# Kernel optimization log

Hardware: AMD Instinct MI355X
Metric: run time of the kernel (lower is better)

## Reference

```python
import jax, jax.numpy as jnp
import numpy as np

FEAT_STRIDE = 16
SCALES = np.array([8.0, 16.0, 32.0])
RATIOS = np.array([0.5, 1.0, 2.0])
PRE_NMS_TOP_N = 6000
POST_NMS_TOP_N = 300
NMS_THRESH = 0.7


def _whctrs(anchor):
    w = anchor[2] - anchor[0] + 1.0
    h = anchor[3] - anchor[1] + 1.0
    cx = anchor[0] + 0.5 * (w - 1.0)
    cy = anchor[1] + 0.5 * (h - 1.0)
    return w, h, cx, cy


def _mkanchors(ws, hs, cx, cy):
    return np.stack([cx - 0.5 * (ws - 1.0), cy - 0.5 * (hs - 1.0),
                     cx + 0.5 * (ws - 1.0), cy + 0.5 * (hs - 1.0)], axis=1)


def generate_anchors(base_size=16, ratios=RATIOS, scales=SCALES):
    base = np.array([0.0, 0.0, base_size - 1.0, base_size - 1.0])
    w, h, cx, cy = _whctrs(base)
    size = w * h
    ws = np.round(np.sqrt(size / ratios))
    hs = np.round(ws * ratios)
    ratio_anchors = _mkanchors(ws, hs, cx, cy)
    out = []
    for a in ratio_anchors:
        w, h, cx, cy = _whctrs(a)
        out.append(_mkanchors(w * scales, h * scales, cx, cy))
    return np.vstack(out)  # (A=9, 4)


def setup_inputs():
    key = jax.random.key(0)
    k1, k2 = jax.random.split(key)
    B, A, H, W = 8, 9, 152, 152
    scores_in = jax.random.normal(k1, (B, 2 * A, H, W), jnp.float32)
    bbox_deltas = 0.5 * jax.random.normal(k2, (B, 4 * A, H, W), jnp.float32)
    im_info = jnp.tile(jnp.array([[H * FEAT_STRIDE, W * FEAT_STRIDE, 1.0]], jnp.float32), (B, 1))
    anchors = jnp.asarray(generate_anchors(), jnp.float32)
    return {"scores_in": scores_in, "bbox_deltas": bbox_deltas, "im_info": im_info, "anchors": anchors}


def bbox_transform_inv(boxes, deltas):
    w = boxes[..., 2] - boxes[..., 0] + 1.0
    h = boxes[..., 3] - boxes[..., 1] + 1.0
    cx = boxes[..., 0] + 0.5 * w
    cy = boxes[..., 1] + 0.5 * h
    dx, dy, dw, dh = deltas[..., 0], deltas[..., 1], deltas[..., 2], deltas[..., 3]
    pcx = dx * w + cx
    pcy = dy * h + cy
    pw = jnp.exp(dw) * w
    ph = jnp.exp(dh) * h
    return jnp.stack([pcx - 0.5 * pw, pcy - 0.5 * ph, pcx + 0.5 * pw, pcy + 0.5 * ph], axis=-1)


def clip_boxes(boxes, im_info):
    wmax = im_info[:, None, 1] - 1.0  # x bound, per image
    hmax = im_info[:, None, 0] - 1.0  # y bound
    x1 = jnp.minimum(jnp.maximum(boxes[..., 0], 0.0), wmax)
    y1 = jnp.minimum(jnp.maximum(boxes[..., 1], 0.0), hmax)
    x2 = jnp.minimum(jnp.maximum(boxes[..., 2], 0.0), wmax)
    y2 = jnp.minimum(jnp.maximum(boxes[..., 3], 0.0), hmax)
    return jnp.stack([x1, y1, x2, y2], axis=-1)


def nms_indices(boxes, thresh, max_out):
    # boxes: (N, 4), sorted by score descending. Greedy NMS -> up to max_out indices, -1 padded.
    x1, y1, x2, y2 = boxes[:, 0], boxes[:, 1], boxes[:, 2], boxes[:, 3]
    areas = (x2 - x1 + 1.0) * (y2 - y1 + 1.0)
    N = boxes.shape[0]

    def body(i, carry):
        suppressed, keep = carry
        idx = jnp.argmax(~suppressed)  # first surviving box = highest remaining score
        valid = ~suppressed[idx]
        keep = keep.at[i].set(jnp.where(valid, idx.astype(jnp.int32), -1))
        xx1 = jnp.maximum(x1[idx], x1)
        yy1 = jnp.maximum(y1[idx], y1)
        xx2 = jnp.minimum(x2[idx], x2)
        yy2 = jnp.minimum(y2[idx], y2)
        inter = jnp.maximum(xx2 - xx1 + 1.0, 0.0) * jnp.maximum(yy2 - yy1 + 1.0, 0.0)
        iou = inter / (areas[idx] + areas - inter)
        suppressed = jnp.where(valid, suppressed | (iou > thresh), suppressed)
        return suppressed, keep

    _, keep = jax.lax.fori_loop(0, max_out, body,
                                (jnp.zeros(N, bool), jnp.full(max_out, -1, jnp.int32)))
    return keep


def _forward(scores_in, bbox_deltas, im_info, anchors):
    B, _, H, W = scores_in.shape
    A = anchors.shape[0]
    # fg objectness scores: channels [A:2A] -> (B, K*A) in (row, col, anchor) order
    scores = scores_in[:, A:].transpose(0, 2, 3, 1).reshape(B, -1)
    deltas = bbox_deltas.transpose(0, 2, 3, 1).reshape(B, -1, 4)
    sx = (jnp.arange(W) * FEAT_STRIDE).astype(jnp.float32)
    sy = (jnp.arange(H) * FEAT_STRIDE).astype(jnp.float32)
    gx, gy = jnp.meshgrid(sx, sy)  # (H, W)
    shifts = jnp.stack([gx.ravel(), gy.ravel(), gx.ravel(), gy.ravel()], axis=1)  # (K, 4)
    all_anchors = (anchors[None, :, :] + shifts[:, None, :]).reshape(-1, 4)  # (K*A, 4)
    proposals = bbox_transform_inv(all_anchors[None], deltas)  # (B, K*A, 4)
    proposals = clip_boxes(proposals, im_info)
    _, order = jax.lax.top_k(scores, PRE_NMS_TOP_N)  # descending, == sorted order truncated
    props_top = jnp.take_along_axis(proposals, order[..., None], axis=1)  # (B, PRE, 4)
    keep = jax.vmap(lambda b: nms_indices(b, NMS_THRESH, POST_NMS_TOP_N))(props_top)  # (B, POST)
    valid = keep >= 0
    sel = jnp.take_along_axis(props_top, jnp.maximum(keep, 0)[..., None], axis=1)
    sel = jnp.where(valid[..., None], sel, 0.0)
    batch_col = jnp.broadcast_to(jnp.arange(B, dtype=jnp.float32)[:, None, None],
                                 (B, POST_NMS_TOP_N, 1))
    return jnp.concatenate([batch_col, sel], axis=2)  # (B, POST, 5)


def reference(scores_in, bbox_deltas, im_info, anchors):
    return _forward(scores_in, bbox_deltas, im_info, anchors)
```

## Files before the change

### kernel.cpp

```cpp
#include <hip/hip_runtime.h>
#include <stdint.h>

#define H_ 152
#define W_ 152
#define A_ 9
#define HW_ (H_ * W_)
#define N_ (HW_ * A_)
#define B_ 8
#define PRE_TOP 6000
#define POST_TOP 300
#define NBUCK 4096
#define NFINE 32768
#define CAND_CAP 8192
#define NMS_TH 0.7f
#define CNT_STRIDE 32
#define RTILE 512
#define DEC_PIXBLK 91
#define DEC_BLKS (72 * DEC_PIXBLK)
#define ZERO_BLKS 128

#define OFF_HIST    0
#define OFF_SSUF    131072
#define OFF_CNT     262144
#define OFF_CAND    263168
#define OFF_GROUP   787456
#define OFF_BOXES   1311744
#define OFF_BALL    2079744
#define WS_NEED     (2079744ull + 26615808ull)


__device__ __forceinline__ unsigned fkey(float f) {
    unsigned u = __float_as_uint(f);
    return (u & 0x80000000u) ? ~u : (u | 0x80000000u);
}

__device__ __forceinline__ bool sup_test(float ax1, float ay1, float ax2, float ay2, float aar,
                                         float bx1, float by1, float bx2, float by2, float bar) {
    float xx1 = fmaxf(ax1, bx1);
    float yy1 = fmaxf(ay1, by1);
    float xx2 = fminf(ax2, bx2);
    float yy2 = fminf(ay2, by2);
    float iw = fmaxf(xx2 - xx1 + 1.0f, 0.0f);
    float ih = fmaxf(yy2 - yy1 + 1.0f, 0.0f);
    float inter = __fmul_rn(iw, ih);
    float iou = inter / (aar + bar - inter);
    return iou > NMS_TH;
}

__device__ __forceinline__ float4 decode_box(float an0, float an1, float an2, float an3,
                                             float sx, float sy,
                                             float dx, float dy, float dw, float dh,
                                             float wmax, float hmax) {
    float ax1 = an0 + sx;
    float ay1 = an1 + sy;
    float ax2 = an2 + sx;
    float ay2 = an3 + sy;
    float ww = ax2 - ax1 + 1.0f;
    float hh = ay2 - ay1 + 1.0f;
    float ctx = ax1 + 0.5f * ww;
    float cty = ay1 + 0.5f * hh;
    float pcx = __fadd_rn(__fmul_rn(dx, ww), ctx);
    float pcy = __fadd_rn(__fmul_rn(dy, hh), cty);
    float pw = __fmul_rn(expf(dw), ww);
    float ph = __fmul_rn(expf(dh), hh);
    float x1 = pcx - 0.5f * pw;
    float y1 = pcy - 0.5f * ph;
    float x2 = pcx + 0.5f * pw;
    float y2 = pcy + 0.5f * ph;
    x1 = fminf(fmaxf(x1, 0.0f), wmax);
    y1 = fminf(fmaxf(y1, 0.0f), hmax);
    x2 = fminf(fmaxf(x2, 0.0f), wmax);
    y2 = fminf(fmaxf(y2, 0.0f), hmax);
    return make_float4(x1, y1, x2, y2);
}


__global__ void init_k(const float* __restrict__ deltas,
                       const float* __restrict__ anchors,
                       const float* __restrict__ im_info,
                       float4* __restrict__ ball,
                       unsigned* __restrict__ zbase, unsigned* __restrict__ zboxes,
                       int nDecBlks) {
    int bid = blockIdx.x;
    if (bid < nDecBlks) {
        int ba = bid / DEC_PIXBLK;
        int b = ba / A_, a = ba - (ba / A_) * A_;
        int pix = (bid % DEC_PIXBLK) * 256 + threadIdx.x;
        if (pix >= HW_) return;
        const float* db = deltas + ((size_t)b * 36 + 4 * a) * HW_;
        float dx = db[pix];
        float dy = db[pix + HW_];
        float dw = db[pix + 2 * HW_];
        float dh = db[pix + 3 * HW_];
        float an0 = anchors[a * 4 + 0];
        float an1 = anchors[a * 4 + 1];
        float an2 = anchors[a * 4 + 2];
        float an3 = anchors[a * 4 + 3];
        float hmax = im_info[b * 3 + 0] - 1.0f;
        float wmax = im_info[b * 3 + 1] - 1.0f;
        int w = pix % W_, h = pix / W_;
        float sx = (float)(w * 16), sy = (float)(h * 16);
        ball[(size_t)b * N_ + a * HW_ + pix] =
            decode_box(an0, an1, an2, an3, sx, sy, dx, dy, dw, dh, wmax, hmax);
    } else {
        const int n1 = 263168 / 4;
        const int n2 = 768000 / 4;
        int i = (bid - nDecBlks) * 256 + (int)threadIdx.x;
        int st = ZERO_BLKS * 256;
        for (int k = i; k < n1 + n2; k += st) {
            if (k < n1) zbase[k] = 0u;
            else zboxes[k - n1] = 0u;
        }
    }
}

__global__ void hist_k(const float* __restrict__ scores, unsigned* __restrict__ hist) {
    __shared__ unsigned lh[NBUCK];
    int b = blockIdx.y;
    for (int i = threadIdx.x; i < NBUCK; i += blockDim.x) lh[i] = 0;
    __syncthreads();
    const float4* sb = (const float4*)(scores + ((size_t)b * 18 + A_) * HW_);
    const int N4 = N_ / 4;
    int stride = gridDim.x * blockDim.x;
    for (int e = blockIdx.x * blockDim.x + threadIdx.x; e < N4; e += stride) {
        float4 v = sb[e];
        atomicAdd(&lh[fkey(v.x) >> 20], 1u);
        atomicAdd(&lh[fkey(v.y) >> 20], 1u);
        atomicAdd(&lh[fkey(v.z) >> 20], 1u);
        atomicAdd(&lh[fkey(v.w) >> 20], 1u);
    }
    __syncthreads();
    for (int i = threadIdx.x; i < NBUCK; i += blockDim.x) {
        unsigned v = lh[i];
        if (v) atomicAdd(&hist[b * NBUCK + i], v);
    }
}

__global__ void scan_k(const unsigned* __restrict__ hist, unsigned* __restrict__ bucketT) {
    __shared__ unsigned ps[1024];
    int b = blockIdx.x, t = threadIdx.x;
    const unsigned* hb = hist + b * NBUCK;
    unsigned c0 = hb[4095 - (4 * t + 0)];
    unsigned c1 = hb[4095 - (4 * t + 1)];
    unsigned c2 = hb[4095 - (4 * t + 2)];
    unsigned c3 = hb[4095 - (4 * t + 3)];
    unsigned local = c0 + c1 + c2 + c3;
    ps[t] = local;
    __syncthreads();
    for (int off = 1; off < 1024; off <<= 1) {
        unsigned v = (t >= off) ? ps[t - off] : 0u;
        __syncthreads();
        ps[t] += v;
        __syncthreads();
    }
    unsigned incl = ps[t], excl = incl - local;
    if (excl < PRE_TOP && incl >= PRE_TOP) {
        unsigned cum = excl;
        unsigned cc[4] = {c0, c1, c2, c3};
#pragma unroll
        for (int k = 0; k < 4; ++k) {
            cum += cc[k];
            if (cum >= PRE_TOP) { bucketT[b] = (unsigned)(4095 - (4 * t + k)); break; }
        }
    }
    if (t == 1023 && ps[1023] < PRE_TOP) bucketT[b] = 0;
}

__global__ void compact_k(const float* __restrict__ scores, const unsigned* __restrict__ bucketT,
                          unsigned* __restrict__ cnt, uint2* __restrict__ cand) {
    __shared__ unsigned wtot[4], wbase[4];
    __shared__ unsigned blkbase;
    int b = blockIdx.y;
    const float4* sb = (const float4*)(scores + ((size_t)b * 18 + A_) * HW_);
    unsigned T = bucketT[b];
    int lane = threadIdx.x & 63;
    int wid = threadIdx.x >> 6;
    const int N4 = N_ / 4;
    int stride = gridDim.x * blockDim.x;
    int niters = (N4 + stride - 1) / stride;
    unsigned long long lower = (lane == 63) ? 0x7fffffffffffffffull
                                            : ((1ull << lane) - 1ull);
    for (int it = 0; it < niters; ++it) {
        int e = it * stride + blockIdx.x * (int)blockDim.x + (int)threadIdx.x;
        bool p0 = false, p1 = false, p2 = false, p3 = false;
        unsigned k0 = 0, k1 = 0, k2 = 0, k3 = 0;
        if (e < N4) {
            float4 v = sb[e];
            k0 = fkey(v.x); k1 = fkey(v.y); k2 = fkey(v.z); k3 = fkey(v.w);
            p0 = (k0 >> 20) >= T; p1 = (k1 >> 20) >= T;
            p2 = (k2 >> 20) >= T; p3 = (k3 >> 20) >= T;
        }
        unsigned long long m0 = __ballot(p0), m1 = __ballot(p1);
        unsigned long long m2 = __ballot(p2), m3 = __ballot(p3);
        unsigned t0 = (unsigned)__popcll(m0), t1 = (unsigned)__popcll(m1);
        unsigned t2 = (unsigned)__popcll(m2), t3 = (unsigned)__popcll(m3);
        unsigned wtotal = t0 + t1 + t2 + t3;
        if (lane == 0) wtot[wid] = wtotal;
        __syncthreads();
        if (threadIdx.x == 0) {
            unsigned s0 = wtot[0], s1 = wtot[1], s2 = wtot[2], s3 = wtot[3];
            unsigned tot = s0 + s1 + s2 + s3;
            blkbase = tot ? atomicAdd(&cnt[b * CNT_STRIDE], tot) : 0u;
            wbase[0] = 0; wbase[1] = s0; wbase[2] = s0 + s1; wbase[3] = s0 + s1 + s2;
        }
        __syncthreads();
        if (wtotal) {
            unsigned base = blkbase + wbase[wid];
            unsigned o0 = base + (unsigned)__popcll(m0 & lower);
            unsigned o1 = base + t0 + (unsigned)__popcll(m1 & lower);
            unsigned o2 = base + t0 + t1 + (unsigned)__popcll(m2 & lower);
            unsigned o3 = base + t0 + t1 + t2 + (unsigned)__popcll(m3 & lower);
            uint2* cb = cand + (size_t)b * CAND_CAP;
            int e4 = e * 4;
            if (p0 && o0 < CAND_CAP) {
                int a = (e4 + 0) / HW_, pix = (e4 + 0) - a * HW_;
                cb[o0] = make_uint2(k0, (unsigned)(pix * A_ + a));
            }
            if (p1 && o1 < CAND_CAP) {
                int a = (e4 + 1) / HW_, pix = (e4 + 1) - a * HW_;
                cb[o1] = make_uint2(k1, (unsigned)(pix * A_ + a));
            }
            if (p2 && o2 < CAND_CAP) {
                int a = (e4 + 2) / HW_, pix = (e4 + 2) - a * HW_;
                cb[o2] = make_uint2(k2, (unsigned)(pix * A_ + a));
            }
            if (p3 && o3 < CAND_CAP) {
                int a = (e4 + 3) / HW_, pix = (e4 + 3) - a * HW_;
                cb[o3] = make_uint2(k3, (unsigned)(pix * A_ + a));
            }
        }
    }
}

__global__ void __launch_bounds__(1024) finesort_k(const unsigned* __restrict__ cnt,
                                                   uint2* __restrict__ cand,
                                                   unsigned long long* __restrict__ grouped) {
    __shared__ unsigned lh[NFINE];
    __shared__ unsigned ps[1024];
    int b = blockIdx.x, t = threadIdx.x;
    int M = min((int)cnt[b * CNT_STRIDE], CAND_CAP);
    uint2* cb = cand + (size_t)b * CAND_CAP;
    unsigned long long* g = grouped + (size_t)b * CAND_CAP;
    for (int i = t; i < NFINE; i += 1024) lh[i] = 0u;
    __syncthreads();
    for (int i = t; i < M; i += 1024) {
        unsigned key16 = cb[i].x >> 16;
        unsigned f = (key16 >= 32768u) ? (key16 - 32768u) : 0u;
        atomicAdd(&lh[f], 1u);
    }
    __syncthreads();
    unsigned c[32];
    unsigned local = 0;
#pragma unroll
    for (int k = 0; k < 32; ++k) { c[k] = lh[32767 - (32 * t + k)]; local += c[k]; }
    ps[t] = local;
    __syncthreads();
    for (int off = 1; off < 1024; off <<= 1) {
        unsigned v = (t >= off) ? ps[t - off] : 0u;
        __syncthreads();
        ps[t] += v;
        __syncthreads();
    }
    unsigned run = ps[t] - local;
    __syncthreads();
#pragma unroll
    for (int k = 0; k < 32; ++k) {
        lh[32767 - (32 * t + k)] = run;
        run += c[k];
    }
    __syncthreads();
    for (int i = t; i < M; i += 1024) {
        uint2 cd = cb[i];
        unsigned key16 = cd.x >> 16;
        unsigned f = (key16 >= 32768u) ? (key16 - 32768u) : 0u;
        unsigned pos = atomicAdd(&lh[f], 1u);
        if (pos < CAND_CAP)
            g[pos] = ((unsigned long long)cd.x << 32) | (unsigned)(~cd.y);
    }
    __syncthreads();
    ushort* S16 = (ushort*)cb;
    for (int i = t; i < NFINE; i += 1024)
        S16[i] = (ushort)min(lh[i], 65535u);
}

__global__ void __launch_bounds__(256) rank_k(const unsigned* __restrict__ cnt,
                                              const unsigned long long* __restrict__ grouped,
                                              const ushort* __restrict__ S16all,
                                              const float* __restrict__ deltas,
                                              const float* __restrict__ anchors,
                                              const float* __restrict__ im_info,
                                              const float4* __restrict__ ball,
                                              float4* __restrict__ boxes) {
    __shared__ unsigned long long tile[RTILE];
    __shared__ int s_rs, s_re;
    int b = blockIdx.y, t = threadIdx.x;
    int M = min((int)cnt[b * CNT_STRIDE], CAND_CAP);
    int c0 = blockIdx.x * 256;
    if (c0 >= M) return;
    const unsigned long long* g = grouped + (size_t)b * CAND_CAP;
    const ushort* S16 = S16all + (size_t)b * NFINE;
    int i = c0 + t;
    bool valid = i < M;
    unsigned long long comp = valid ? g[i] : 0ull;

    unsigned n = valid ? ~(unsigned)comp : 0u;
    int a = (int)(n % A_);
    int pix = (int)(n / A_);

    float4 pre = make_float4(0.f, 0.f, 0.f, 0.f);
    float dx = 0.f, dy = 0.f, dw = 0.f, dh = 0.f;
    float an0 = 0.f, an1 = 0.f, an2 = 0.f, an3 = 0.f, hmax = 0.f, wmax = 0.f;
    if (ball) {
        if (valid) pre = ball[(size_t)b * N_ + a * HW_ + pix];
    } else if (valid) {
        const float* db = deltas + (size_t)b * 36 * HW_;
        int didx = (4 * a) * HW_ + pix;
        dx = db[didx];
        dy = db[didx + HW_];
        dw = db[didx + 2 * HW_];
        dh = db[didx + 3 * HW_];
        an0 = anchors[a * 4 + 0];
        an1 = anchors[a * 4 + 1];
        an2 = anchors[a * 4 + 2];
        an3 = anchors[a * 4 + 3];
        hmax = im_info[b * 3 + 0] - 1.0f;
        wmax = im_info[b * 3 + 1] - 1.0f;
    }

    unsigned key16 = (unsigned)(comp >> 48);
    int f = (key16 >= 32768u) ? (int)(key16 - 32768u) : 0;
    int bs = 0, be = 0;
    if (valid) {
        bs = (f < 32767) ? min((int)S16[f + 1], M) : 0;
        be = min((int)S16[f], M);
    }
    if (t == 0) {
        unsigned kf = (unsigned)(g[c0] >> 48);
        int bf = (kf >= 32768u) ? (int)(kf - 32768u) : 0;
        int last = min(c0 + 255, M - 1);
        unsigned kl = (unsigned)(g[last] >> 48);
        int bl = (kl >= 32768u) ? (int)(kl - 32768u) : 0;
        s_rs = (bf < 32767) ? min((int)S16[bf + 1], M) : 0;
        s_re = min((int)S16[bl], M);
    }
    __syncthreads();
    int rs = s_rs, re = s_re;
    int cgt = 0;
    for (int tb = rs; tb < re; tb += RTILE) {
        int navail = min(RTILE, re - tb);
        __syncthreads();
        for (int j = t; j < navail; j += 256) tile[j] = g[tb + j];
        __syncthreads();
        if (valid) {
            int lo = max(bs, tb) - tb;
            int hi = min(be, tb + navail) - tb;
            int a0 = 0, a1 = 0, a2 = 0, a3 = 0, a4 = 0, a5 = 0, a6 = 0, a7 = 0;
            int j = lo;
            for (; j + 8 <= hi; j += 8) {
                unsigned long long v0 = tile[j + 0];
                unsigned long long v1 = tile[j + 1];
                unsigned long long v2 = tile[j + 2];
                unsigned long long v3 = tile[j + 3];
                unsigned long long v4 = tile[j + 4];
                unsigned long long v5 = tile[j + 5];
                unsigned long long v6 = tile[j + 6];
                unsigned long long v7 = tile[j + 7];
                a0 += (v0 > comp); a1 += (v1 > comp); a2 += (v2 > comp); a3 += (v3 > comp);
                a4 += (v4 > comp); a5 += (v5 > comp); a6 += (v6 > comp); a7 += (v7 > comp);
            }
            for (; j < hi; ++j) cgt += (tile[j] > comp);
            cgt += (a0 + a1 + a2 + a3) + (a4 + a5 + a6 + a7);
        }
    }
    if (!valid) return;
    int rank = bs + cgt;
    if (rank >= PRE_TOP) return;

    float4 result;
    if (ball) {
        result = pre;
    } else {
        int w = pix % W_, h = pix / W_;
        float sx = (float)(w * 16), sy = (float)(h * 16);
        result = decode_box(an0, an1, an2, an3, sx, sy, dx, dy, dw, dh, wmax, hmax);
    }
    boxes[(size_t)b * PRE_TOP + rank] = result;
}

__global__ void __launch_bounds__(1024) nms_k(const float4* __restrict__ boxes,
                                              float* __restrict__ out) {
    __shared__ float4 kbox[POST_TOP];
    __shared__ float  karea[POST_TOP];
    __shared__ float4 gbox4[64];
    __shared__ float  gar[64];
    __shared__ unsigned extw[2];
    __shared__ unsigned intraw[128];
    __shared__ unsigned long long s_keep;
    __shared__ int s_base, s_kc, s_done;
    int b = blockIdx.x, t = threadIdx.x;
    int lane = t & 63, w = t >> 6;
    if (t == 0) { s_kc = 0; s_done = 0; }
    const float4* bb = boxes + (size_t)b * PRE_TOP;
    const int ngroups = (PRE_TOP + 63) / 64;

    float4 vcur = make_float4(0.f, 0.f, 0.f, 0.f);
    if (t < 64) vcur = bb[t];

    for (int g = 0; g < ngroups; ++g) {
        __syncthreads();
        if (s_done) break;
        int gbase = g * 64;
        int gsz = min(64, PRE_TOP - gbase);
        if (t < gsz) {
            gbox4[t] = vcur;
            gar[t] = __fmul_rn(vcur.z - vcur.x + 1.0f, vcur.w - vcur.y + 1.0f);
        }
        if (t < 64) {
            int nidx = min(gbase + 64 + t, PRE_TOP - 1);
            vcur = bb[nidx];
        }
        if (t < 2) extw[t] = 0u;
        if (t < 128) intraw[t] = 0u;
        __syncthreads();

        int kc = s_kc;
        {
            int j = t >> 4, sub = t & 15;
            if (j < gsz) {
                float4 cb4 = gbox4[j];
                float car = gar[j];
                bool any = false;
                for (int kk = sub; kk < kc && !any; kk += 16) {
                    float4 kb = kbox[kk];
                    float ka = karea[kk];
                    any = sup_test(kb.x, kb.y, kb.z, kb.w, ka,
                                   cb4.x, cb4.y, cb4.z, cb4.w, car);
                }
                if (any) atomicOr(&extw[j >> 5], 1u << (j & 31));
            }
        }
        {
            float4 mb = gbox4[lane];
            float mar = gar[lane];
#pragma unroll
            for (int it = 0; it < 4; ++it) {
                int jj = w + it * 16;
                float4 bj = gbox4[jj];
                float baj = gar[jj];
                bool sup = (jj < lane) && (lane < gsz) && (jj < gsz) &&
                           sup_test(bj.x, bj.y, bj.z, bj.w, baj,
                                    mb.x, mb.y, mb.z, mb.w, mar);
                unsigned long long m = __ballot(sup);
                if (lane == 0 && (unsigned)m) atomicOr(&intraw[2 * jj], (unsigned)m);
                if (lane == 1 && (unsigned)(m >> 32))
                    atomicOr(&intraw[2 * jj + 1], (unsigned)(m >> 32));
            }
        }
        __syncthreads();

        if (t == 0) {
            unsigned long long ext64 = (unsigned long long)extw[0] |
                                       ((unsigned long long)extw[1] << 32);
            unsigned long long validm = (gsz >= 64) ? ~0ull : ((1ull << gsz) - 1ull);
            unsigned long long alive = (~ext64) & validm;
            unsigned long long keep = 0ull;
            int kcc = s_kc;
            s_base = kcc;
            while (alive && kcc < POST_TOP) {
                int j = __ffsll((long long)alive) - 1;
                keep |= (1ull << j);
                ++kcc;
                unsigned long long row = (unsigned long long)intraw[2 * j] |
                                         ((unsigned long long)intraw[2 * j + 1] << 32);
                alive &= ~row;
                alive &= ~(1ull << j);
            }
            s_keep = keep;
            s_kc = kcc;
            if (kcc >= POST_TOP) s_done = 1;
        }
        __syncthreads();

        if (t < gsz && ((s_keep >> t) & 1ull)) {
            int rank = __popcll(s_keep & ((1ull << t) - 1ull));
            int slot = s_base + rank;
            float4 mb = gbox4[t];
            kbox[slot] = mb;
            karea[slot] = gar[t];
            float* o = out + (size_t)(b * POST_TOP + slot) * 5;
            o[0] = (float)b; o[1] = mb.x; o[2] = mb.y; o[3] = mb.z; o[4] = mb.w;
        }
    }
    __syncthreads();
    for (int sl = s_kc + t; sl < POST_TOP; sl += 1024) {
        float* o = out + (size_t)(b * POST_TOP + sl) * 5;
        o[0] = (float)b; o[1] = 0.f; o[2] = 0.f; o[3] = 0.f; o[4] = 0.f;
    }
}


extern "C" void kernel_launch(void* const* d_in, const int* in_sizes, int n_in,
                              void* d_out, int out_size, void* d_ws, size_t ws_size,
                              hipStream_t stream) {
    const float* scores  = (const float*)d_in[0];
    const float* deltas  = (const float*)d_in[1];
    const float* im_info = (const float*)d_in[2];
    const float* anchors = (const float*)d_in[3];
    float* out = (float*)d_out;

    unsigned*           hist    = (unsigned*)((char*)d_ws + OFF_HIST);
    unsigned*           cnt     = (unsigned*)((char*)d_ws + OFF_CNT);
    uint2*              cand    = (uint2*)((char*)d_ws + OFF_CAND);
    unsigned long long* grouped = (unsigned long long*)((char*)d_ws + OFF_GROUP);
    float4*             boxes   = (float4*)((char*)d_ws + OFF_BOXES);
    unsigned*           bucketT = cnt + B_ * CNT_STRIDE - 8;

    bool useBall = ws_size >= WS_NEED;
    float4* ball = useBall ? (float4*)((char*)d_ws + OFF_BALL) : nullptr;

    int nDec = useBall ? DEC_BLKS : 0;
    init_k<<<nDec + ZERO_BLKS, 256, 0, stream>>>(deltas, anchors, im_info, ball,
                                                 (unsigned*)d_ws,
                                                 (unsigned*)((char*)d_ws + OFF_BOXES), nDec);
    hist_k<<<dim3(64, B_), 256, 0, stream>>>(scores, hist);
    scan_k<<<B_, 1024, 0, stream>>>(hist, bucketT);
    compact_k<<<dim3(64, B_), 256, 0, stream>>>(scores, bucketT, cnt, cand);
    finesort_k<<<B_, 1024, 0, stream>>>(cnt, cand, grouped);
    rank_k<<<dim3(32, B_), 256, 0, stream>>>(cnt, grouped, (const ushort*)cand,
                                             deltas, anchors, im_info, ball, boxes);
    nms_k<<<B_, 1024, 0, stream>>>(boxes, out);
}
```

Baseline: 93.59 us.

## Decode boxes only for compacted candidates instead of all anchors

Removes the full-image box decode pass that wrote every anchor's box (about 26 MB) to workspace. Boxes are now decoded only for candidates that pass the histogram threshold, inside compact_k, and stored in a per-candidate buffer. finesort_k records each sorted slot's original candidate index so rank_k can gather the precomputed box. This trades a large streaming decode and write for scattered delta reads inside compaction, and reuses the histogram region for the slot map.

```diff
diff --git a/kernel.cpp b/kernel.cpp
--- a/kernel.cpp
+++ b/kernel.cpp
@@ -15,9 +15,6 @@
 #define NMS_TH 0.7f
 #define CNT_STRIDE 32
 #define RTILE 512
-#define DEC_PIXBLK 91
-#define DEC_BLKS (72 * DEC_PIXBLK)
-#define ZERO_BLKS 128
 
 #define OFF_HIST    0
 #define OFF_SSUF    131072
@@ -25,8 +22,8 @@
 #define OFF_CAND    263168
 #define OFF_GROUP   787456
 #define OFF_BOXES   1311744
-#define OFF_BALL    2079744
-#define WS_NEED     (2079744ull + 26615808ull)
+#define OFF_CANDBOX 2079744
+#define WS_NEED     (2079744ull + 1048576ull)
 
 
 __device__ __forceinline__ unsigned fkey(float f) {
@@ -75,42 +72,14 @@
 }
 
 
-__global__ void init_k(const float* __restrict__ deltas,
-                       const float* __restrict__ anchors,
-                       const float* __restrict__ im_info,
-                       float4* __restrict__ ball,
-                       unsigned* __restrict__ zbase, unsigned* __restrict__ zboxes,
-                       int nDecBlks) {
-    int bid = blockIdx.x;
-    if (bid < nDecBlks) {
-        int ba = bid / DEC_PIXBLK;
-        int b = ba / A_, a = ba - (ba / A_) * A_;
-        int pix = (bid % DEC_PIXBLK) * 256 + threadIdx.x;
-        if (pix >= HW_) return;
-        const float* db = deltas + ((size_t)b * 36 + 4 * a) * HW_;
-        float dx = db[pix];
-        float dy = db[pix + HW_];
-        float dw = db[pix + 2 * HW_];
-        float dh = db[pix + 3 * HW_];
-        float an0 = anchors[a * 4 + 0];
-        float an1 = anchors[a * 4 + 1];
-        float an2 = anchors[a * 4 + 2];
-        float an3 = anchors[a * 4 + 3];
-        float hmax = im_info[b * 3 + 0] - 1.0f;
-        float wmax = im_info[b * 3 + 1] - 1.0f;
-        int w = pix % W_, h = pix / W_;
-        float sx = (float)(w * 16), sy = (float)(h * 16);
-        ball[(size_t)b * N_ + a * HW_ + pix] =
-            decode_box(an0, an1, an2, an3, sx, sy, dx, dy, dw, dh, wmax, hmax);
-    } else {
-        const int n1 = 263168 / 4;
-        const int n2 = 768000 / 4;
-        int i = (bid - nDecBlks) * 256 + (int)threadIdx.x;
-        int st = ZERO_BLKS * 256;
-        for (int k = i; k < n1 + n2; k += st) {
-            if (k < n1) zbase[k] = 0u;
-            else zboxes[k - n1] = 0u;
-        }
+__global__ void zero2_k(unsigned* __restrict__ base, unsigned* __restrict__ p2) {
+    const int n1 = 263168 / 4;
+    const int n2 = 768000 / 4;
+    int i = blockIdx.x * blockDim.x + threadIdx.x;
+    int st = gridDim.x * blockDim.x;
+    for (int k = i; k < n1 + n2; k += st) {
+        if (k < n1) base[k] = 0u;
+        else p2[k - n1] = 0u;
     }
 }
 
@@ -166,12 +135,18 @@
     if (t == 1023 && ps[1023] < PRE_TOP) bucketT[b] = 0;
 }
 
-__global__ void compact_k(const float* __restrict__ scores, const unsigned* __restrict__ bucketT,
-                          unsigned* __restrict__ cnt, uint2* __restrict__ cand) {
+__global__ void compact_k(const float* __restrict__ scores, const float* __restrict__ deltas,
+                          const float* __restrict__ anchors, const float* __restrict__ im_info,
+                          const unsigned* __restrict__ bucketT,
+                          unsigned* __restrict__ cnt, uint2* __restrict__ cand,
+                          float4* __restrict__ candbox) {
     __shared__ unsigned wtot[4], wbase[4];
     __shared__ unsigned blkbase;
     int b = blockIdx.y;
     const float4* sb = (const float4*)(scores + ((size_t)b * 18 + A_) * HW_);
+    const float* db = deltas + (size_t)b * 36 * HW_;
+    float hmax = im_info[b * 3 + 0] - 1.0f;
+    float wmax = im_info[b * 3 + 1] - 1.0f;
     unsigned T = bucketT[b];
     int lane = threadIdx.x & 63;
     int wid = threadIdx.x >> 6;
@@ -180,6 +155,8 @@
     int niters = (N4 + stride - 1) / stride;
     unsigned long long lower = (lane == 63) ? 0x7fffffffffffffffull
                                             : ((1ull << lane) - 1ull);
+    uint2* cb = cand + (size_t)b * CAND_CAP;
+    float4* cx = candbox + (size_t)b * CAND_CAP;
     for (int it = 0; it < niters; ++it) {
         int e = it * stride + blockIdx.x * (int)blockDim.x + (int)threadIdx.x;
         bool p0 = false, p1 = false, p2 = false, p3 = false;
@@ -210,37 +187,42 @@
             unsigned o1 = base + t0 + (unsigned)__popcll(m1 & lower);
             unsigned o2 = base + t0 + t1 + (unsigned)__popcll(m2 & lower);
             unsigned o3 = base + t0 + t1 + t2 + (unsigned)__popcll(m3 & lower);
-            uint2* cb = cand + (size_t)b * CAND_CAP;
             int e4 = e * 4;
-            if (p0 && o0 < CAND_CAP) {
-                int a = (e4 + 0) / HW_, pix = (e4 + 0) - a * HW_;
-                cb[o0] = make_uint2(k0, (unsigned)(pix * A_ + a));
+#define EMIT(P, O, K, IDX)                                                      \
+            if (P && O < CAND_CAP) {                                            \
+                int a = (IDX) / HW_, pix = (IDX) - a * HW_;                     \
+                cb[O] = make_uint2(K, (unsigned)(pix * A_ + a));                \
+                int didx = (4 * a) * HW_ + pix;                                 \
+                float dx = db[didx];                                            \
+                float dy = db[didx + HW_];                                      \
+                float dw = db[didx + 2 * HW_];                                  \
+                float dh = db[didx + 3 * HW_];                                  \
+                int w = pix % W_, h = pix / W_;                                 \
+                cx[O] = decode_box(anchors[a * 4 + 0], anchors[a * 4 + 1],      \
+                                   anchors[a * 4 + 2], anchors[a * 4 + 3],      \
+                                   (float)(w * 16), (float)(h * 16),            \
+                                   dx, dy, dw, dh, wmax, hmax);                 \
             }
-            if (p1 && o1 < CAND_CAP) {
-                int a = (e4 + 1) / HW_, pix = (e4 + 1) - a * HW_;
-                cb[o1] = make_uint2(k1, (unsigned)(pix * A_ + a));
-            }
-            if (p2 && o2 < CAND_CAP) {
-                int a = (e4 + 2) / HW_, pix = (e4 + 2) - a * HW_;
-                cb[o2] = make_uint2(k2, (unsigned)(pix * A_ + a));
-            }
-            if (p3 && o3 < CAND_CAP) {
-                int a = (e4 + 3) / HW_, pix = (e4 + 3) - a * HW_;
-                cb[o3] = make_uint2(k3, (unsigned)(pix * A_ + a));
-            }
+            EMIT(p0, o0, k0, e4 + 0)
+            EMIT(p1, o1, k1, e4 + 1)
+            EMIT(p2, o2, k2, e4 + 2)
+            EMIT(p3, o3, k3, e4 + 3)
+#undef EMIT
         }
     }
 }
 
 __global__ void __launch_bounds__(1024) finesort_k(const unsigned* __restrict__ cnt,
                                                    uint2* __restrict__ cand,
-                                                   unsigned long long* __restrict__ grouped) {
+                                                   unsigned long long* __restrict__ grouped,
+                                                   ushort* __restrict__ slot16all) {
     __shared__ unsigned lh[NFINE];
     __shared__ unsigned ps[1024];
     int b = blockIdx.x, t = threadIdx.x;
     int M = min((int)cnt[b * CNT_STRIDE], CAND_CAP);
     uint2* cb = cand + (size_t)b * CAND_CAP;
     unsigned long long* g = grouped + (size_t)b * CAND_CAP;
+    ushort* slot16 = slot16all + (size_t)b * CAND_CAP;
     for (int i = t; i < NFINE; i += 1024) lh[i] = 0u;
     __syncthreads();
     for (int i = t; i < M; i += 1024) {
@@ -274,8 +256,10 @@
         unsigned key16 = cd.x >> 16;
         unsigned f = (key16 >= 32768u) ? (key16 - 32768u) : 0u;
         unsigned pos = atomicAdd(&lh[f], 1u);
-        if (pos < CAND_CAP)
+        if (pos < CAND_CAP) {
             g[pos] = ((unsigned long long)cd.x << 32) | (unsigned)(~cd.y);
+            slot16[pos] = (ushort)i;
+        }
     }
     __syncthreads();
     ushort* S16 = (ushort*)cb;
@@ -286,10 +270,8 @@
 __global__ void __launch_bounds__(256) rank_k(const unsigned* __restrict__ cnt,
                                               const unsigned long long* __restrict__ grouped,
                                               const ushort* __restrict__ S16all,
-                                              const float* __restrict__ deltas,
-                                              const float* __restrict__ anchors,
-                                              const float* __restrict__ im_info,
-                                              const float4* __restrict__ ball,
+                                              const ushort* __restrict__ slot16all,
+                                              const float4* __restrict__ candbox,
                                               float4* __restrict__ boxes) {
     __shared__ unsigned long long tile[RTILE];
     __shared__ int s_rs, s_re;
@@ -299,33 +281,14 @@
     if (c0 >= M) return;
     const unsigned long long* g = grouped + (size_t)b * CAND_CAP;
     const ushort* S16 = S16all + (size_t)b * NFINE;
+    const ushort* slot16 = slot16all + (size_t)b * CAND_CAP;
+    const float4* cx = candbox + (size_t)b * CAND_CAP;
     int i = c0 + t;
     bool valid = i < M;
     unsigned long long comp = valid ? g[i] : 0ull;
 
-    unsigned n = valid ? ~(unsigned)comp : 0u;
-    int a = (int)(n % A_);
-    int pix = (int)(n / A_);
-
     float4 pre = make_float4(0.f, 0.f, 0.f, 0.f);
-    float dx = 0.f, dy = 0.f, dw = 0.f, dh = 0.f;
-    float an0 = 0.f, an1 = 0.f, an2 = 0.f, an3 = 0.f, hmax = 0.f, wmax = 0.f;
-    if (ball) {
-        if (valid) pre = ball[(size_t)b * N_ + a * HW_ + pix];
-    } else if (valid) {
-        const float* db = deltas + (size_t)b * 36 * HW_;
-        int didx = (4 * a) * HW_ + pix;
-        dx = db[didx];
-        dy = db[didx + HW_];
-        dw = db[didx + 2 * HW_];
-        dh = db[didx + 3 * HW_];
-        an0 = anchors[a * 4 + 0];
-        an1 = anchors[a * 4 + 1];
-        an2 = anchors[a * 4 + 2];
-        an3 = anchors[a * 4 + 3];
-        hmax = im_info[b * 3 + 0] - 1.0f;
-        wmax = im_info[b * 3 + 1] - 1.0f;
-    }
+    if (valid) pre = cx[slot16[i]];
 
     unsigned key16 = (unsigned)(comp >> 48);
     int f = (key16 >= 32768u) ? (int)(key16 - 32768u) : 0;
@@ -375,16 +338,7 @@
     if (!valid) return;
     int rank = bs + cgt;
     if (rank >= PRE_TOP) return;
-
-    float4 result;
-    if (ball) {
-        result = pre;
-    } else {
-        int w = pix % W_, h = pix / W_;
-        float sx = (float)(w * 16), sy = (float)(h * 16);
-        result = decode_box(an0, an1, an2, an3, sx, sy, dx, dy, dw, dh, wmax, hmax);
-    }
-    boxes[(size_t)b * PRE_TOP + rank] = result;
+    boxes[(size_t)b * PRE_TOP + rank] = pre;
 }
 
 __global__ void __launch_bounds__(1024) nms_k(const float4* __restrict__ boxes,
@@ -513,20 +467,17 @@
     uint2*              cand    = (uint2*)((char*)d_ws + OFF_CAND);
     unsigned long long* grouped = (unsigned long long*)((char*)d_ws + OFF_GROUP);
     float4*             boxes   = (float4*)((char*)d_ws + OFF_BOXES);
+    float4*             candbox = (float4*)((char*)d_ws + OFF_CANDBOX);
+    ushort*             slot16  = (ushort*)((char*)d_ws + OFF_HIST);
     unsigned*           bucketT = cnt + B_ * CNT_STRIDE - 8;
 
-    bool useBall = ws_size >= WS_NEED;
-    float4* ball = useBall ? (float4*)((char*)d_ws + OFF_BALL) : nullptr;
-
-    int nDec = useBall ? DEC_BLKS : 0;
-    init_k<<<nDec + ZERO_BLKS, 256, 0, stream>>>(deltas, anchors, im_info, ball,
-                                                 (unsigned*)d_ws,
-                                                 (unsigned*)((char*)d_ws + OFF_BOXES), nDec);
+    zero2_k<<<128, 256, 0, stream>>>((unsigned*)d_ws, (unsigned*)((char*)d_ws + OFF_BOXES));
     hist_k<<<dim3(64, B_), 256, 0, stream>>>(scores, hist);
     scan_k<<<B_, 1024, 0, stream>>>(hist, bucketT);
-    compact_k<<<dim3(64, B_), 256, 0, stream>>>(scores, bucketT, cnt, cand);
-    finesort_k<<<B_, 1024, 0, stream>>>(cnt, cand, grouped);
+    compact_k<<<dim3(64, B_), 256, 0, stream>>>(scores, deltas, anchors, im_info,
+                                                bucketT, cnt, cand, candbox);
+    finesort_k<<<B_, 1024, 0, stream>>>(cnt, cand, grouped, slot16);
     rank_k<<<dim3(32, B_), 256, 0, stream>>>(cnt, grouped, (const ushort*)cand,
-                                             deltas, anchors, im_info, ball, boxes);
+                                             slot16, candbox, boxes);
     nms_k<<<B_, 1024, 0, stream>>>(boxes, out);
 }
```

Measured after the change: 98.31 us. +5.0%, slower.
